# Kernel tuning notes

Measured on AMD Instinct MI355X. Metric: run time of the kernel, lower is better.

## Reference

```python
import jax, jax.numpy as jnp
import numpy as np

B, T, DIM = 32, 512, 512
Q, C, D = 8, 256, 256   # num_codebooks, nb_code, bottleneck_dim
HID = 1024
EPS = 1e-5


def _bn(h, gamma, beta):
    # BatchNorm1d (training mode): batch stats over all leading dims, biased var
    ax = tuple(range(h.ndim - 1))
    m = h.mean(axis=ax, keepdims=True)
    v = ((h - m) ** 2).mean(axis=ax, keepdims=True)
    return (h - m) / jnp.sqrt(v + EPS) * gamma + beta


def setup_inputs() -> dict:
    key = jax.random.key(0)
    ks = jax.random.split(key, 12)
    s = 0.02  # weight scale
    return {
        "x": jax.random.normal(ks[0], (B, DIM, T), jnp.float32),
        "u": jax.random.uniform(ks[1], (B, T, Q, C), jnp.float32),
        "codebook": jax.random.normal(ks[2], (Q, C, D), jnp.float32),
        "log_temps": jnp.zeros((Q,), jnp.float32),
        "enc_w0": jax.random.normal(ks[3], (HID, DIM), jnp.float32) * s,
        "enc_b0": jnp.zeros((HID,), jnp.float32),
        "enc_g0": jnp.ones((HID,), jnp.float32),
        "enc_be0": jnp.zeros((HID,), jnp.float32),
        "enc_w1": jax.random.normal(ks[4], (HID, HID), jnp.float32) * s,
        "enc_b1": jnp.zeros((HID,), jnp.float32),
        "enc_g1": jnp.ones((HID,), jnp.float32),
        "enc_be1": jnp.zeros((HID,), jnp.float32),
        "enc_wo": jax.random.normal(ks[5], (Q * D, HID), jnp.float32) * s,
        "enc_bo": jnp.zeros((Q * D,), jnp.float32),
        "dec_g": jnp.ones((D,), jnp.float32),
        "dec_be": jnp.zeros((D,), jnp.float32),
        "dec_w0": jax.random.normal(ks[6], (HID, D), jnp.float32) * s,
        "dec_b0": jnp.zeros((HID,), jnp.float32),
        "dec_g0": jnp.ones((HID,), jnp.float32),
        "dec_be0": jnp.zeros((HID,), jnp.float32),
        "dec_w1": jax.random.normal(ks[7], (HID, HID), jnp.float32) * s,
        "dec_b1": jnp.zeros((HID,), jnp.float32),
        "dec_g1": jnp.ones((HID,), jnp.float32),
        "dec_be1": jnp.zeros((HID,), jnp.float32),
        "fin_w": jax.random.normal(ks[8], (DIM, HID), jnp.float32) * s,
        "fin_b": jnp.zeros((DIM,), jnp.float32),
    }


def reference(x, u, codebook, log_temps,
              enc_w0, enc_b0, enc_g0, enc_be0,
              enc_w1, enc_b1, enc_g1, enc_be1,
              enc_wo, enc_bo,
              dec_g, dec_be,
              dec_w0, dec_b0, dec_g0, dec_be0,
              dec_w1, dec_b1, dec_g1, dec_be1,
              fin_w, fin_b):
    xt = jnp.swapaxes(x, 1, 2)  # b c t -> b t c

    # encoder: FFN(dim->hid->hid) + Linear(hid, Q*D)
    h = jax.nn.relu(_bn(xt @ enc_w0.T + enc_b0, enc_g0, enc_be0))
    h = jax.nn.relu(_bn(h @ enc_w1.T + enc_b1, enc_g1, enc_be1))
    z = (h @ enc_wo.T + enc_bo).reshape(B, T, Q, D)

    # multi-codebook logits
    logits_raw = jnp.einsum('btqd,qcd->btqc', z, codebook)  # [B,T,Q,C]
    indices = jnp.argmax(logits_raw, axis=-1)               # [B,T,Q]

    # per-codebook temperature scaling
    logits = logits_raw * jnp.exp(-log_temps)[:, None]

    # gumbel-softmax (tau=1, hard=True), gumbel noise from uniform u
    g = -jnp.log(-jnp.log(jnp.clip(u, 1e-9, 1.0)) + 1e-20)
    y_soft = jax.nn.softmax(logits + g, axis=-1)
    y_hard = jax.nn.one_hot(jnp.argmax(y_soft, axis=-1), C, dtype=y_soft.dtype)
    codes = y_hard - jax.lax.stop_gradient(y_soft) + y_soft  # straight-through

    # decoder: embed via codebook, batchnorm, FFN, final linear
    emb = codes.reshape(B, T, Q * C) @ codebook.reshape(Q * C, D)
    h = _bn(emb, dec_g, dec_be)
    h = jax.nn.relu(_bn(h @ dec_w0.T + dec_b0, dec_g0, dec_be0))
    h = jax.nn.relu(_bn(h @ dec_w1.T + dec_b1, dec_g1, dec_be1))
    x_reco = h @ fin_w.T + fin_b  # [B,T,DIM]

    commit_loss = jnp.mean((x_reco - xt) ** 2)
    return x_reco, indices, commit_loss
```

## Files before the change

kernel.cpp:

```cpp
#include <hip/hip_runtime.h>
#include <math.h>

#define BB   32
#define TT   512
#define DIM  512
#define HID  1024
#define QQ   8
#define CC   256
#define DD   256
#define BT   16384
#define EPSB 1e-5f

typedef _Float16 half4 __attribute__((ext_vector_type(4)));
typedef _Float16 half8 __attribute__((ext_vector_type(8)));
typedef float f32x4 __attribute__((ext_vector_type(4)));

#define GLOAD_LDS16(g, l)                                                      \
  __builtin_amdgcn_global_load_lds(                                            \
      (const __attribute__((address_space(1))) void*)(g),                      \
      (__attribute__((address_space(3))) void*)(l), 16, 0, 0)

#define S_BARRIER() asm volatile("s_barrier" ::: "memory")
#define S_VMCNT8()  asm volatile("s_waitcnt vmcnt(8)" ::: "memory")
#define S_VMCNT4()  asm volatile("s_waitcnt vmcnt(4)" ::: "memory")
#define S_VMCNT0()  asm volatile("s_waitcnt vmcnt(0)" ::: "memory")

__device__ inline void xcd_swizzle(int& bx, int& by) {
  int gx = gridDim.x, gy = gridDim.y;
  int h = blockIdx.x + gx * blockIdx.y;
  int c = h & 7, idx = h >> 3;
  bx = idx % gx;
  by = c * (gy >> 3) + idx / gx;
}

__global__ __launch_bounds__(256) void transpose_xt(const float* __restrict__ x,
                                                    float* __restrict__ xt,
                                                    _Float16* __restrict__ xhi,
                                                    _Float16* __restrict__ xlo) {
  __shared__ float tile[32][33];
  int tx = threadIdx.x, ty = threadIdx.y;
  int b = blockIdx.z;
  int t0 = blockIdx.x * 32, c0 = blockIdx.y * 32;
  const float* xb = x + (size_t)b * DIM * TT;
#pragma unroll
  for (int j = 0; j < 32; j += 8)
    tile[ty + j][tx] = xb[(size_t)(c0 + ty + j) * TT + (t0 + tx)];
  __syncthreads();
#pragma unroll
  for (int j = 0; j < 32; j += 8) {
    float v = tile[tx][ty + j];
    size_t gi = ((size_t)b * TT + t0 + ty + j) * DIM + (c0 + tx);
    xt[gi] = v;
    _Float16 h = (_Float16)v;
    xhi[gi] = h;
    xlo[gi] = (_Float16)(v - (float)h);
  }
}

__device__ inline void conv4(const float* __restrict__ in,
                             _Float16* __restrict__ o, int i) {
  float4 v = ((const float4*)in)[i];
  half4 hv;
  hv.x = (_Float16)v.x; hv.y = (_Float16)v.y;
  hv.z = (_Float16)v.z; hv.w = (_Float16)v.w;
  ((half4*)o)[i] = hv;
}

__device__ inline void split4(const float* __restrict__ in,
                              _Float16* __restrict__ hi,
                              _Float16* __restrict__ lo, int i, float scale) {
  float4 v = ((const float4*)in)[i];
  v.x *= scale; v.y *= scale; v.z *= scale; v.w *= scale;
  half4 hv, lv;
  hv.x = (_Float16)v.x; lv.x = (_Float16)(v.x - (float)hv.x);
  hv.y = (_Float16)v.y; lv.y = (_Float16)(v.y - (float)hv.y);
  hv.z = (_Float16)v.z; lv.z = (_Float16)(v.z - (float)hv.z);
  hv.w = (_Float16)v.w; lv.w = (_Float16)(v.w - (float)hv.w);
  ((half4*)hi)[i] = hv;
  ((half4*)lo)[i] = lv;
}

__global__ __launch_bounds__(256) void prep_weights(
    const float* __restrict__ dw0, const float* __restrict__ dw1,
    const float* __restrict__ fw, const float* __restrict__ ew0,
    const float* __restrict__ ew1, _Float16* __restrict__ w0h,
    _Float16* __restrict__ w1h, _Float16* __restrict__ wfh,
    _Float16* __restrict__ w0hi, _Float16* __restrict__ w0lo,
    _Float16* __restrict__ w1hi, _Float16* __restrict__ w1lo) {
  int b = blockIdx.x, t = threadIdx.x;
  if (b < 256) {
    conv4(dw0, w0h, b * 256 + t);
  } else if (b < 1280) {
    conv4(dw1, w1h, (b - 256) * 256 + t);
  } else if (b < 1792) {
    conv4(fw, wfh, (b - 1280) * 256 + t);
  } else if (b < 2304) {
    split4(ew0, w0hi, w0lo, (b - 1792) * 256 + t, 64.f);
  } else {
    split4(ew1, w1hi, w1lo, (b - 2304) * 256 + t, 64.f);
  }
}

__global__ __launch_bounds__(256) void fold_w(const float* __restrict__ cb,
                                              const float* __restrict__ wo,
                                              float* __restrict__ Wf) {
  __shared__ float As[8][128];
  __shared__ float Ws[8][128];
  const int tid = threadIdx.x;
  const int n0 = blockIdx.x * 128;
  const int m0 = blockIdx.y * 128;
  const int q = m0 >> 8;
  const int lr = tid >> 1, lk = (tid & 1) << 2;
  const float* Ap = cb + (size_t)q * CC * DD + (size_t)((m0 & 255) + lr) * DD + lk;
  const int br = tid >> 5, bc = (tid & 31) << 2;
  const float* Bp = wo + (size_t)(q * CC + br) * HID + n0 + bc;
  const int tm = (tid >> 4) << 3, tn = (tid & 15) << 3;

  float acc[8][8];
#pragma unroll
  for (int i = 0; i < 8; i++)
#pragma unroll
    for (int j = 0; j < 8; j++) acc[i][j] = 0.f;

  for (int kb = 0; kb < DD; kb += 8) {
    float4 av = *(const float4*)(Ap + kb);
    float4 bb = *(const float4*)(Bp + (size_t)kb * HID);
    __syncthreads();
    As[lk + 0][lr] = av.x; As[lk + 1][lr] = av.y;
    As[lk + 2][lr] = av.z; As[lk + 3][lr] = av.w;
    *(float4*)&Ws[br][bc] = bb;
    __syncthreads();
#pragma unroll
    for (int k = 0; k < 8; ++k) {
      float a[8], b[8];
      *(float4*)(a) = *(const float4*)(&As[k][tm]);
      *(float4*)(a + 4) = *(const float4*)(&As[k][tm + 4]);
      *(float4*)(b) = *(const float4*)(&Ws[k][tn]);
      *(float4*)(b + 4) = *(const float4*)(&Ws[k][tn + 4]);
#pragma unroll
      for (int i = 0; i < 8; i++)
#pragma unroll
        for (int j = 0; j < 8; j++) acc[i][j] = fmaf(a[i], b[j], acc[i][j]);
    }
  }
#pragma unroll
  for (int i = 0; i < 8; i++) {
    float* Cp = Wf + (size_t)(m0 + tm + i) * HID + (n0 + tn);
    float4 o;
    o.x = acc[i][0]; o.y = acc[i][1]; o.z = acc[i][2]; o.w = acc[i][3];
    *(float4*)Cp = o;
    o.x = acc[i][4]; o.y = acc[i][5]; o.z = acc[i][6]; o.w = acc[i][7];
    *(float4*)(Cp + 4) = o;
  }
}

__global__ __launch_bounds__(256) void fold_b(const float* __restrict__ cb,
                                              const float* __restrict__ bo,
                                              float* __restrict__ bf) {
  int q = blockIdx.x, c = threadIdx.x;
  const float* row = cb + ((size_t)q * CC + c) * DD;
  const float* b = bo + q * DD;
  float s = 0.f;
  for (int d = 0; d < DD; d++) s = fmaf(row[d], b[d], s);
  bf[q * CC + c] = s;
}

__global__ __launch_bounds__(256, 2) void hgemm3s_nt(
    const _Float16* __restrict__ Ahi, const _Float16* __restrict__ Alo,
    const _Float16* __restrict__ Whi, const _Float16* __restrict__ Wlo,
    const float* __restrict__ bias, float invsc, _Float16* __restrict__ Chi,
    _Float16* __restrict__ Clo, int ldc, int K, float* __restrict__ stats,
    int N) {
  __shared__ _Float16 Ah[2][4 * 128 * 8];
  __shared__ _Float16 Al[2][4 * 128 * 8];
  __shared__ _Float16 Bh[2][4 * 128 * 8];
  __shared__ _Float16 Bl[2][4 * 128 * 8];
  int BX, BY;
  xcd_swizzle(BX, BY);
  const int tid = threadIdx.x;
  const int l = tid & 63;
  const int w = tid >> 6;
  const int m0 = BY * 128, n0 = BX * 128;
  const int wrow = (w >> 1) * 64, wcol = (w & 1) * 64;

  const int s0 = tid, s1 = tid + 256;
  const int r0 = s0 & 127, kp0 = s0 >> 7;
  const int r1 = s1 & 127, kp1 = s1 >> 7;
  const size_t a0o = (size_t)(m0 + r0) * K + kp0 * 8;
  const size_t a1o = (size_t)(m0 + r1) * K + kp1 * 8;
  const size_t w0o = (size_t)(n0 + r0) * K + kp0 * 8;
  const size_t w1o = (size_t)(n0 + r1) * K + kp1 * 8;

  f32x4 acc[4][4] = {};

  auto stage = [&](int buf, int kb) {
    GLOAD_LDS16(Ahi + a0o + kb, &Ah[buf][s0 * 8]);
    GLOAD_LDS16(Ahi + a1o + kb, &Ah[buf][s1 * 8]);
    GLOAD_LDS16(Alo + a0o + kb, &Al[buf][s0 * 8]);
    GLOAD_LDS16(Alo + a1o + kb, &Al[buf][s1 * 8]);
    GLOAD_LDS16(Whi + w0o + kb, &Bh[buf][s0 * 8]);
    GLOAD_LDS16(Whi + w1o + kb, &Bh[buf][s1 * 8]);
    GLOAD_LDS16(Wlo + w0o + kb, &Bl[buf][s0 * 8]);
    GLOAD_LDS16(Wlo + w1o + kb, &Bl[buf][s1 * 8]);
  };
  auto compute = [&](int buf) {
    half8 ah[4], al[4], bh[4], bl[4];
#pragma unroll
    for (int i = 0; i < 4; i++) {
      const int idx = (((l >> 4) << 7) + wrow + i * 16 + (l & 15)) * 8;
      ah[i] = *(const half8*)&Ah[buf][idx];
      al[i] = *(const half8*)&Al[buf][idx];
    }
#pragma unroll
    for (int j = 0; j < 4; j++) {
      const int idx = (((l >> 4) << 7) + wcol + j * 16 + (l & 15)) * 8;
      bh[j] = *(const half8*)&Bh[buf][idx];
      bl[j] = *(const half8*)&Bl[buf][idx];
    }
#pragma unroll
    for (int i = 0; i < 4; i++)
#pragma unroll
      for (int j = 0; j < 4; j++) {
        acc[i][j] = __builtin_amdgcn_mfma_f32_16x16x32_f16(ah[i], bh[j],
                                                           acc[i][j], 0, 0, 0);
        acc[i][j] = __builtin_amdgcn_mfma_f32_16x16x32_f16(al[i], bh[j],
                                                           acc[i][j], 0, 0, 0);
        acc[i][j] = __builtin_amdgcn_mfma_f32_16x16x32_f16(ah[i], bl[j],
                                                           acc[i][j], 0, 0, 0);
      }
  };

  stage(0, 0);
  int cur = 0;
  for (int kb = 32; kb < K; kb += 32) {
    stage(cur ^ 1, kb);
    S_VMCNT8();
    S_BARRIER();
    compute(cur);
    S_BARRIER();
    cur ^= 1;
  }
  S_VMCNT0();
  S_BARRIER();
  compute(cur);

#pragma unroll
  for (int j = 0; j < 4; j++) {
    const int col = n0 + wcol + j * 16 + (l & 15);
    const float bb = bias[col];
    float s1v = 0.f, s2v = 0.f;
#pragma unroll
    for (int i = 0; i < 4; i++) {
#pragma unroll
      for (int r = 0; r < 4; r++) {
        float v = fmaf(acc[i][j][r], invsc, bb);
        const int row = m0 + wrow + i * 16 + ((l >> 4) << 2) + r;
        _Float16 hv = (_Float16)v;
        Chi[(size_t)row * ldc + col] = hv;
        Clo[(size_t)row * ldc + col] = (_Float16)(v - (float)hv);
        s1v += v;
        s2v = fmaf(v, v, s2v);
      }
    }
    s1v += __shfl_xor(s1v, 16); s1v += __shfl_xor(s1v, 32);
    s2v += __shfl_xor(s2v, 16); s2v += __shfl_xor(s2v, 32);
    if (l < 16) {
      atomicAdd(&stats[col], s1v);
      atomicAdd(&stats[N + col], s2v);
    }
  }
}

__global__ __launch_bounds__(512, 4) void hgemm3_wo_argmax(
    const _Float16* __restrict__ Ahi, const _Float16* __restrict__ Alo,
    const _Float16* __restrict__ Whi, const _Float16* __restrict__ Wlo,
    const float* __restrict__ bf, const float* __restrict__ u,
    const float* __restrict__ log_temps, float* __restrict__ out_idx,
    int* __restrict__ idx2) {
  __shared__ _Float16 Ahs[4 * 128 * 8];
  __shared__ _Float16 Als[4 * 128 * 8];
  __shared__ _Float16 Bhs[4 * 256 * 8];
  __shared__ _Float16 Bls[4 * 256 * 8];
  __shared__ float redv[2][128][4];
  __shared__ int   redi[2][128][4];
  int BX, BY;
  xcd_swizzle(BX, BY);
  const int tid = threadIdx.x;
  const int l = tid & 63;
  const int w = tid >> 6;
  const int q = BX;
  const int m0 = BY * 128;
  const int n0 = q * CC;
  const int wrow = (w >> 2) * 64, wcol = (w & 3) * 64;

  const int ar = tid & 127, akp = tid >> 7;
  const _Float16* Agh = Ahi + (size_t)(m0 + ar) * HID + akp * 8;
  const _Float16* Agl = Alo + (size_t)(m0 + ar) * HID + akp * 8;
  _Float16* Ahd = &Ahs[tid * 8];
  _Float16* Ald = &Als[tid * 8];
  const int s0 = tid, s1 = tid + 512;
  const int br0 = s0 & 255, bkp0 = s0 >> 8;
  const int br1 = s1 & 255, bkp1 = s1 >> 8;
  const _Float16* Bgh0 = Whi + (size_t)(n0 + br0) * HID + bkp0 * 8;
  const _Float16* Bgh1 = Whi + (size_t)(n0 + br1) * HID + bkp1 * 8;
  const _Float16* Bgl0 = Wlo + (size_t)(n0 + br0) * HID + bkp0 * 8;
  const _Float16* Bgl1 = Wlo + (size_t)(n0 + br1) * HID + bkp1 * 8;
  _Float16* Bhd0 = &Bhs[s0 * 8]; _Float16* Bhd1 = &Bhs[s1 * 8];
  _Float16* Bld0 = &Bls[s0 * 8]; _Float16* Bld1 = &Bls[s1 * 8];

  f32x4 acc[4][4] = {};

  for (int kb = 0; kb < HID; kb += 32) {
    __syncthreads();
    GLOAD_LDS16(Agh + kb, Ahd);
    GLOAD_LDS16(Agl + kb, Ald);
    GLOAD_LDS16(Bgh0 + kb, Bhd0);
    GLOAD_LDS16(Bgh1 + kb, Bhd1);
    GLOAD_LDS16(Bgl0 + kb, Bld0);
    GLOAD_LDS16(Bgl1 + kb, Bld1);
    __syncthreads();
    half8 ah[4], al[4], bh[4], bl[4];
#pragma unroll
    for (int i = 0; i < 4; i++) {
      const int idx = ((l >> 4) * 128 + wrow + i * 16 + (l & 15)) * 8;
      ah[i] = *(const half8*)&Ahs[idx];
      al[i] = *(const half8*)&Als[idx];
    }
#pragma unroll
    for (int j = 0; j < 4; j++) {
      const int idx = ((l >> 4) * 256 + wcol + j * 16 + (l & 15)) * 8;
      bh[j] = *(const half8*)&Bhs[idx];
      bl[j] = *(const half8*)&Bls[idx];
    }
#pragma unroll
    for (int i = 0; i < 4; i++)
#pragma unroll
      for (int j = 0; j < 4; j++) {
        acc[i][j] = __builtin_amdgcn_mfma_f32_16x16x32_f16(ah[i], bh[j],
                                                           acc[i][j], 0, 0, 0);
        acc[i][j] = __builtin_amdgcn_mfma_f32_16x16x32_f16(al[i], bh[j],
                                                           acc[i][j], 0, 0, 0);
        acc[i][j] = __builtin_amdgcn_mfma_f32_16x16x32_f16(ah[i], bl[j],
                                                           acc[i][j], 0, 0, 0);
      }
  }

  const float scale = expf(-log_temps[q]);
  float bcol[4];
#pragma unroll
  for (int j = 0; j < 4; j++) bcol[j] = bf[n0 + wcol + j * 16 + (l & 15)];

#pragma unroll
  for (int i = 0; i < 4; i++) {
#pragma unroll
    for (int r = 0; r < 4; r++) {
      const int rloc = wrow + i * 16 + ((l >> 4) << 2) + r;
      const int row = m0 + rloc;
      float bvv = -INFINITY; int bi = 0;
      float gv = -INFINITY; int gi = 0;
#pragma unroll
      for (int j = 0; j < 4; j++) {
        const int c = wcol + j * 16 + (l & 15);
        float v = acc[i][j][r] + bcol[j];
        if (v > bvv) { bvv = v; bi = c; }
        float uu = u[(size_t)row * (QQ * CC) + n0 + c];
        float uc = fminf(fmaxf(uu, 1e-9f), 1.0f);
        float g = -logf(-logf(uc) + 1e-20f);
        float y = fmaf(v, scale, g);
        if (y > gv) { gv = y; gi = c; }
      }
#pragma unroll
      for (int off = 1; off < 16; off <<= 1) {
        float b2 = __shfl_xor(bvv, off); int bi2 = __shfl_xor(bi, off);
        if (b2 > bvv || (b2 == bvv && bi2 < bi)) { bvv = b2; bi = bi2; }
        float g2 = __shfl_xor(gv, off); int gi2 = __shfl_xor(gi, off);
        if (g2 > gv || (g2 == gv && gi2 < gi)) { gv = g2; gi = gi2; }
      }
      if ((l & 15) == 0) {
        redv[0][rloc][w & 3] = bvv; redi[0][rloc][w & 3] = bi;
        redv[1][rloc][w & 3] = gv;  redi[1][rloc][w & 3] = gi;
      }
    }
  }
  __syncthreads();
  if (tid < 128) {
    float bv = redv[0][tid][0]; int bi = redi[0][tid][0];
    float gv = redv[1][tid][0]; int gi = redi[1][tid][0];
#pragma unroll
    for (int c = 1; c < 4; c++) {
      float v = redv[0][tid][c];
      if (v > bv) { bv = v; bi = redi[0][tid][c]; }
      float v2 = redv[1][tid][c];
      if (v2 > gv) { gv = v2; gi = redi[1][tid][c]; }
    }
    const int row = m0 + tid;
    out_idx[(size_t)row * QQ + q] = (float)bi;
    idx2[(size_t)row * QQ + q] = gi;
  }
}

__global__ __launch_bounds__(256, 2) void hgemm_ntf16(
    const _Float16* __restrict__ A, const _Float16* __restrict__ W,
    const float* __restrict__ bias, _Float16* __restrict__ C, int ldc, int K,
    float* __restrict__ stats, int N) {
  __shared__ _Float16 Al[2][4 * 128 * 8];
  __shared__ _Float16 Bl[2][4 * 128 * 8];
  int BX, BY;
  xcd_swizzle(BX, BY);
  const int tid = threadIdx.x;
  const int l = tid & 63;
  const int w = tid >> 6;
  const int m0 = BY * 128, n0 = BX * 128;
  const int wrow = (w >> 1) * 64, wcol = (w & 1) * 64;

  const int s0 = tid, s1 = tid + 256;
  const int r0 = s0 & 127, kp0 = s0 >> 7;
  const int r1 = s1 & 127, kp1 = s1 >> 7;
  const size_t a0o = (size_t)(m0 + r0) * K + kp0 * 8;
  const size_t a1o = (size_t)(m0 + r1) * K + kp1 * 8;
  const size_t w0o = (size_t)(n0 + r0) * K + kp0 * 8;
  const size_t w1o = (size_t)(n0 + r1) * K + kp1 * 8;

  f32x4 acc[4][4] = {};

  auto stage = [&](int buf, int kb) {
    GLOAD_LDS16(A + a0o + kb, &Al[buf][s0 * 8]);
    GLOAD_LDS16(A + a1o + kb, &Al[buf][s1 * 8]);
    GLOAD_LDS16(W + w0o + kb, &Bl[buf][s0 * 8]);
    GLOAD_LDS16(W + w1o + kb, &Bl[buf][s1 * 8]);
  };
  auto compute = [&](int buf) {
    half8 af[4], bfr[4];
#pragma unroll
    for (int i = 0; i < 4; i++)
      af[i] = *(const half8*)
          &Al[buf][(((l >> 4) << 7) + wrow + i * 16 + (l & 15)) * 8];
#pragma unroll
    for (int j = 0; j < 4; j++)
      bfr[j] = *(const half8*)
          &Bl[buf][(((l >> 4) << 7) + wcol + j * 16 + (l & 15)) * 8];
#pragma unroll
    for (int i = 0; i < 4; i++)
#pragma unroll
      for (int j = 0; j < 4; j++)
        acc[i][j] = __builtin_amdgcn_mfma_f32_16x16x32_f16(af[i], bfr[j],
                                                           acc[i][j], 0, 0, 0);
  };

  stage(0, 0);
  int cur = 0;
  for (int kb = 32; kb < K; kb += 32) {
    stage(cur ^ 1, kb);
    S_VMCNT4();
    S_BARRIER();
    compute(cur);
    S_BARRIER();
    cur ^= 1;
  }
  S_VMCNT0();
  S_BARRIER();
  compute(cur);

#pragma unroll
  for (int j = 0; j < 4; j++) {
    const int col = n0 + wcol + j * 16 + (l & 15);
    const float bb = bias[col];
    float s1v = 0.f, s2v = 0.f;
#pragma unroll
    for (int i = 0; i < 4; i++) {
#pragma unroll
      for (int r = 0; r < 4; r++) {
        float v = acc[i][j][r] + bb;
        const int row = m0 + wrow + i * 16 + ((l >> 4) << 2) + r;
        C[(size_t)row * ldc + col] = (_Float16)v;
        s1v += v;
        s2v = fmaf(v, v, s2v);
      }
    }
    s1v += __shfl_xor(s1v, 16); s1v += __shfl_xor(s1v, 32);
    s2v += __shfl_xor(s2v, 16); s2v += __shfl_xor(s2v, 32);
    if (l < 16) {
      atomicAdd(&stats[col], s1v);
      atomicAdd(&stats[N + col], s2v);
    }
  }
}

__global__ __launch_bounds__(256, 2) void hgemm_nt_loss(
    const _Float16* __restrict__ A, const _Float16* __restrict__ W,
    const float* __restrict__ bias, float* __restrict__ C, int ldc, int K,
    const float* __restrict__ xt, float* __restrict__ out_loss) {
  __shared__ _Float16 Al[2][4 * 128 * 8];
  __shared__ _Float16 Bl[2][4 * 128 * 8];
  int BX, BY;
  xcd_swizzle(BX, BY);
  const int tid = threadIdx.x;
  const int l = tid & 63;
  const int w = tid >> 6;
  const int m0 = BY * 128, n0 = BX * 128;
  const int wrow = (w >> 1) * 64, wcol = (w & 1) * 64;

  const int s0 = tid, s1 = tid + 256;
  const int r0 = s0 & 127, kp0 = s0 >> 7;
  const int r1 = s1 & 127, kp1 = s1 >> 7;
  const size_t a0o = (size_t)(m0 + r0) * K + kp0 * 8;
  const size_t a1o = (size_t)(m0 + r1) * K + kp1 * 8;
  const size_t w0o = (size_t)(n0 + r0) * K + kp0 * 8;
  const size_t w1o = (size_t)(n0 + r1) * K + kp1 * 8;

  f32x4 acc[4][4] = {};

  auto stage = [&](int buf, int kb) {
    GLOAD_LDS16(A + a0o + kb, &Al[buf][s0 * 8]);
    GLOAD_LDS16(A + a1o + kb, &Al[buf][s1 * 8]);
    GLOAD_LDS16(W + w0o + kb, &Bl[buf][s0 * 8]);
    GLOAD_LDS16(W + w1o + kb, &Bl[buf][s1 * 8]);
  };
  auto compute = [&](int buf) {
    half8 af[4], bfr[4];
#pragma unroll
    for (int i = 0; i < 4; i++)
      af[i] = *(const half8*)
          &Al[buf][(((l >> 4) << 7) + wrow + i * 16 + (l & 15)) * 8];
#pragma unroll
    for (int j = 0; j < 4; j++)
      bfr[j] = *(const half8*)
          &Bl[buf][(((l >> 4) << 7) + wcol + j * 16 + (l & 15)) * 8];
#pragma unroll
    for (int i = 0; i < 4; i++)
#pragma unroll
      for (int j = 0; j < 4; j++)
        acc[i][j] = __builtin_amdgcn_mfma_f32_16x16x32_f16(af[i], bfr[j],
                                                           acc[i][j], 0, 0, 0);
  };

  stage(0, 0);
  int cur = 0;
  for (int kb = 32; kb < K; kb += 32) {
    stage(cur ^ 1, kb);
    S_VMCNT4();
    S_BARRIER();
    compute(cur);
    S_BARRIER();
    cur ^= 1;
  }
  S_VMCNT0();
  S_BARRIER();
  compute(cur);

  float ls = 0.f;
#pragma unroll
  for (int j = 0; j < 4; j++) {
    const int col = n0 + wcol + j * 16 + (l & 15);
    const float bb = bias[col];
#pragma unroll
    for (int i = 0; i < 4; i++) {
#pragma unroll
      for (int r = 0; r < 4; r++) {
        float v = acc[i][j][r] + bb;
        const int row = m0 + wrow + i * 16 + ((l >> 4) << 2) + r;
        C[(size_t)row * ldc + col] = v;
        float d = v - xt[(size_t)row * ldc + col];
        ls = fmaf(d, d, ls);
      }
    }
  }
#pragma unroll
  for (int off = 32; off > 0; off >>= 1) ls += __shfl_xor(ls, off);
  if (l == 0)
    atomicAdd(out_loss, ls * (1.0f / ((float)BT * (float)DIM)));
}

__global__ __launch_bounds__(256) void bn_finalize(const float* __restrict__ sums,
                                                   const float* __restrict__ gamma,
                                                   const float* __restrict__ beta,
                                                   float* __restrict__ ss, int N) {
  int n = blockIdx.x * 256 + threadIdx.x;
  if (n >= N) return;
  const float invM = 1.0f / (float)BT;
  float mean = sums[n] * invM;
  float var = sums[N + n] * invM - mean * mean;
  float sc = gamma[n] / sqrtf(var + EPSB);
  ss[n] = sc;
  ss[N + n] = beta[n] - mean * sc;
}

__global__ __launch_bounds__(256) void bn_resplit(_Float16* __restrict__ hi,
                                                  _Float16* __restrict__ lo,
                                                  const float* __restrict__ ss,
                                                  int nmask, int N, long n4,
                                                  int relu) {
  long stride = (long)gridDim.x * 256;
  for (long i = (long)blockIdx.x * 256 + threadIdx.x; i < n4; i += stride) {
    int col = (int)((i << 2) & nmask);
    half4 h = ((half4*)hi)[i];
    half4 L = ((half4*)lo)[i];
    float4 sc = *(const float4*)(ss + col);
    float4 sh = *(const float4*)(ss + N + col);
    float vx = fmaf((float)h.x + (float)L.x, sc.x, sh.x);
    float vy = fmaf((float)h.y + (float)L.y, sc.y, sh.y);
    float vz = fmaf((float)h.z + (float)L.z, sc.z, sh.z);
    float vw = fmaf((float)h.w + (float)L.w, sc.w, sh.w);
    if (relu) {
      vx = fmaxf(vx, 0.f); vy = fmaxf(vy, 0.f);
      vz = fmaxf(vz, 0.f); vw = fmaxf(vw, 0.f);
    }
    half4 hv, lv;
    hv.x = (_Float16)vx; lv.x = (_Float16)(vx - (float)hv.x);
    hv.y = (_Float16)vy; lv.y = (_Float16)(vy - (float)hv.y);
    hv.z = (_Float16)vz; lv.z = (_Float16)(vz - (float)hv.z);
    hv.w = (_Float16)vw; lv.w = (_Float16)(vw - (float)hv.w);
    ((half4*)hi)[i] = hv;
    ((half4*)lo)[i] = lv;
  }
}

__global__ __launch_bounds__(256) void bnf16_inplace(_Float16* __restrict__ h,
                                                     const float* __restrict__ ss,
                                                     int nmask, int N, long n4,
                                                     int relu) {
  long stride = (long)gridDim.x * 256;
  for (long i = (long)blockIdx.x * 256 + threadIdx.x; i < n4; i += stride) {
    int col = (int)((i << 2) & nmask);
    half4 v = ((half4*)h)[i];
    float4 sc = *(const float4*)(ss + col);
    float4 sh = *(const float4*)(ss + N + col);
    float vx = fmaf((float)v.x, sc.x, sh.x);
    float vy = fmaf((float)v.y, sc.y, sh.y);
    float vz = fmaf((float)v.z, sc.z, sh.z);
    float vw = fmaf((float)v.w, sc.w, sh.w);
    if (relu) {
      vx = fmaxf(vx, 0.f); vy = fmaxf(vy, 0.f);
      vz = fmaxf(vz, 0.f); vw = fmaxf(vw, 0.f);
    }
    half4 o;
    o.x = (_Float16)vx; o.y = (_Float16)vy;
    o.z = (_Float16)vz; o.w = (_Float16)vw;
    ((half4*)h)[i] = o;
  }
}

__global__ __launch_bounds__(256) void bn_apply_f16(const float* __restrict__ h,
                                                    const float* __restrict__ ss,
                                                    int nmask, int N, long n4,
                                                    int relu,
                                                    _Float16* __restrict__ o) {
  long stride = (long)gridDim.x * 256;
  for (long i = (long)blockIdx.x * 256 + threadIdx.x; i < n4; i += stride) {
    int col = (int)((i << 2) & nmask);
    float4 v = ((const float4*)h)[i];
    float4 sc = *(const float4*)(ss + col);
    float4 sh = *(const float4*)(ss + N + col);
    v.x = fmaf(v.x, sc.x, sh.x); v.y = fmaf(v.y, sc.y, sh.y);
    v.z = fmaf(v.z, sc.z, sh.z); v.w = fmaf(v.w, sc.w, sh.w);
    if (relu) {
      v.x = fmaxf(v.x, 0.f); v.y = fmaxf(v.y, 0.f);
      v.z = fmaxf(v.z, 0.f); v.w = fmaxf(v.w, 0.f);
    }
    half4 hv;
    hv.x = (_Float16)v.x; hv.y = (_Float16)v.y;
    hv.z = (_Float16)v.z; hv.w = (_Float16)v.w;
    ((half4*)o)[i] = hv;
  }
}

__global__ __launch_bounds__(256) void conv_split_s(const float* __restrict__ in,
                                                    _Float16* __restrict__ hi,
                                                    _Float16* __restrict__ lo,
                                                    int n4, float scale) {
  int i = blockIdx.x * 256 + threadIdx.x;
  if (i >= n4) return;
  split4(in, hi, lo, i, scale);
}

__global__ __launch_bounds__(256) void emb_gather_stats(
    const float* __restrict__ cb, const int* __restrict__ idx2,
    float* __restrict__ emb, float* __restrict__ sums) {
  __shared__ int k[64][8];
  const int r0 = blockIdx.x * 64;
  const int tid = threadIdx.x;
  for (int t = tid; t < 64 * QQ; t += 256)
    k[t >> 3][t & 7] = idx2[(size_t)(r0 + (t >> 3)) * QQ + (t & 7)];
  __syncthreads();
  const int d = tid;
  float s1 = 0.f, s2 = 0.f;
  for (int rr = 0; rr < 64; rr++) {
    float s = 0.f;
#pragma unroll
    for (int q = 0; q < QQ; q++)
      s += cb[((size_t)(q * CC + k[rr][q])) * DD + d];
    emb[(size_t)(r0 + rr) * DD + d] = s;
    s1 += s;
    s2 = fmaf(s, s, s2);
  }
  atomicAdd(&sums[d], s1);
  atomicAdd(&sums[DD + d], s2);
}

static const size_t OF_XT = 0;
static const size_t OF_R1 = OF_XT + (size_t)BT * DIM;
static const size_t OF_R2 = OF_R1 + (size_t)BT * HID;
static const size_t OF_WF = OF_R2 + (size_t)BT * HID;
static const size_t OF_BF = OF_WF + (size_t)2048 * HID;
static const size_t OF_EMBH = OF_BF + 2048;
static const size_t OF_HB = OF_EMBH + (size_t)BT * DD / 2;
static const size_t OF_W0H = OF_HB + (size_t)BT * HID / 2;
static const size_t OF_W1H = OF_W0H + (size_t)HID * DD / 2;
static const size_t OF_WFH = OF_W1H + (size_t)HID * HID / 2;
static const size_t OF_I2 = OF_WFH + (size_t)DIM * HID / 2;
static const size_t OF_ST = OF_I2 + (size_t)BT * QQ;
static const size_t OF_SS0 = OF_ST + 4096;
static const size_t OF_SS1 = OF_SS0 + 2048;
static const size_t OF_SSD = OF_SS1 + 2048;
static const size_t OF_SD0 = OF_SSD + 1024;
static const size_t OF_SD1 = OF_SD0 + 2048;

extern "C" void kernel_launch(void* const* d_in, const int* in_sizes, int n_in,
                              void* d_out, int out_size, void* d_ws, size_t ws_size,
                              hipStream_t stream) {
  const float* x        = (const float*)d_in[0];
  const float* u        = (const float*)d_in[1];
  const float* codebook = (const float*)d_in[2];
  const float* log_temps= (const float*)d_in[3];
  const float* enc_w0   = (const float*)d_in[4];
  const float* enc_b0   = (const float*)d_in[5];
  const float* enc_g0   = (const float*)d_in[6];
  const float* enc_be0  = (const float*)d_in[7];
  const float* enc_w1   = (const float*)d_in[8];
  const float* enc_b1   = (const float*)d_in[9];
  const float* enc_g1   = (const float*)d_in[10];
  const float* enc_be1  = (const float*)d_in[11];
  const float* enc_wo   = (const float*)d_in[12];
  const float* enc_bo   = (const float*)d_in[13];
  const float* dec_g    = (const float*)d_in[14];
  const float* dec_be   = (const float*)d_in[15];
  const float* dec_w0   = (const float*)d_in[16];
  const float* dec_b0   = (const float*)d_in[17];
  const float* dec_g0   = (const float*)d_in[18];
  const float* dec_be0  = (const float*)d_in[19];
  const float* dec_w1   = (const float*)d_in[20];
  const float* dec_b1   = (const float*)d_in[21];
  const float* dec_g1   = (const float*)d_in[22];
  const float* dec_be1  = (const float*)d_in[23];
  const float* fin_w    = (const float*)d_in[24];
  const float* fin_b    = (const float*)d_in[25];

  float* ws = (float*)d_ws;
  float* xt = ws + OF_XT;
  float* R1 = ws + OF_R1;
  float* Wf = ws + OF_WF;
  float* bfold = ws + OF_BF;
  _Float16* embh = (_Float16*)(ws + OF_EMBH);
  _Float16* w0h = (_Float16*)(ws + OF_W0H);
  _Float16* w1h = (_Float16*)(ws + OF_W1H);
  _Float16* wfh = (_Float16*)(ws + OF_WFH);
  int* idx2 = (int*)(ws + OF_I2);
  float* st = ws + OF_ST;
  float* ss0 = ws + OF_SS0;
  float* ss1 = ws + OF_SS1;
  float* ssd = ws + OF_SSD;
  float* sd0 = ws + OF_SD0;
  float* sd1 = ws + OF_SD1;

  _Float16* xthi = (_Float16*)(ws + OF_R2);
  _Float16* xtlo = (_Float16*)(ws + OF_R2 + (size_t)BT * DIM / 2);
  _Float16* w0hi = (_Float16*)(ws + OF_R2 + (size_t)BT * DIM);
  _Float16* w0lo = (_Float16*)(ws + OF_R2 + (size_t)BT * DIM + (size_t)HID * DIM / 2);
  _Float16* w1hi = (_Float16*)(ws + OF_R2 + (size_t)BT * DIM + (size_t)HID * DIM);
  _Float16* w1lo = (_Float16*)(ws + OF_R2 + (size_t)BT * DIM + (size_t)HID * DIM +
                               (size_t)HID * HID / 2);
  _Float16* r1hi = (_Float16*)(ws + OF_R1);
  _Float16* r1lo = (_Float16*)(ws + OF_R1 + (size_t)BT * HID / 2);
  _Float16* r2hi = (_Float16*)(ws + OF_HB);
  _Float16* r2lo = (_Float16*)(ws + OF_R2);
  _Float16* wfhi = (_Float16*)(ws + OF_R1);
  _Float16* wflo = (_Float16*)(ws + OF_R1 + (size_t)2048 * HID / 2);
  _Float16* h16a = (_Float16*)(ws + OF_R2);
  _Float16* h16b = (_Float16*)(ws + OF_R2 + (size_t)BT * HID / 2);

  float* out = (float*)d_out;
  float* out_idx = out + (size_t)BT * DIM;
  float* out_loss = out + (size_t)BT * DIM + (size_t)BT * QQ;

  hipMemsetAsync(out_loss, 0, sizeof(float), stream);

  prep_weights<<<dim3(3328), 256, 0, stream>>>(
      dec_w0, dec_w1, fin_w, enc_w0, enc_w1, w0h, w1h, wfh, w0hi, w0lo, w1hi,
      w1lo);
  fold_w<<<dim3(HID / 128, 2048 / 128), 256, 0, stream>>>(codebook, enc_wo, Wf);
  fold_b<<<dim3(QQ), 256, 0, stream>>>(codebook, enc_bo, bfold);

  transpose_xt<<<dim3(TT / 32, DIM / 32, BB), dim3(32, 8), 0, stream>>>(
      x, xt, xthi, xtlo);

  hipMemsetAsync(st, 0, 2 * HID * sizeof(float), stream);
  hgemm3s_nt<<<dim3(HID / 128, BT / 128), 256, 0, stream>>>(
      xthi, xtlo, w0hi, w0lo, enc_b0, 1.f / 64.f, r1hi, r1lo, HID, DIM, st, HID);
  bn_finalize<<<dim3(4), 256, 0, stream>>>(st, enc_g0, enc_be0, ss0, HID);
  bn_resplit<<<dim3(2048), 256, 0, stream>>>(r1hi, r1lo, ss0, HID - 1, HID,
                                             (long)BT * HID / 4, 1);

  hipMemsetAsync(st, 0, 2 * HID * sizeof(float), stream);
  hgemm3s_nt<<<dim3(HID / 128, BT / 128), 256, 0, stream>>>(
      r1hi, r1lo, w1hi, w1lo, enc_b1, 1.f / 64.f, r2hi, r2lo, HID, HID, st, HID);
  conv_split_s<<<dim3(2048 * HID / 4 / 256), 256, 0, stream>>>(
      Wf, wfhi, wflo, 2048 * HID / 4, 1.f);
  bn_finalize<<<dim3(4), 256, 0, stream>>>(st, enc_g1, enc_be1, ss1, HID);
  bn_resplit<<<dim3(2048), 256, 0, stream>>>(r2hi, r2lo, ss1, HID - 1, HID,
                                             (long)BT * HID / 4, 1);

  hgemm3_wo_argmax<<<dim3(QQ, BT / 128), 512, 0, stream>>>(
      r2hi, r2lo, wfhi, wflo, bfold, u, log_temps, out_idx, idx2);

  hipMemsetAsync(st, 0, 2 * DD * sizeof(float), stream);
  emb_gather_stats<<<dim3(BT / 64), 256, 0, stream>>>(codebook, idx2, R1, st);
  bn_finalize<<<dim3(1), 256, 0, stream>>>(st, dec_g, dec_be, ssd, DD);
  bn_apply_f16<<<dim3(2048), 256, 0, stream>>>(R1, ssd, DD - 1, DD,
                                               (long)BT * DD / 4, 0, embh);

  hipMemsetAsync(st, 0, 2 * HID * sizeof(float), stream);
  hgemm_ntf16<<<dim3(HID / 128, BT / 128), 256, 0, stream>>>(
      embh, w0h, dec_b0, h16a, HID, DD, st, HID);
  bn_finalize<<<dim3(4), 256, 0, stream>>>(st, dec_g0, dec_be0, sd0, HID);
  bnf16_inplace<<<dim3(2048), 256, 0, stream>>>(h16a, sd0, HID - 1, HID,
                                                (long)BT * HID / 4, 1);

  hipMemsetAsync(st, 0, 2 * HID * sizeof(float), stream);
  hgemm_ntf16<<<dim3(HID / 128, BT / 128), 256, 0, stream>>>(
      h16a, w1h, dec_b1, h16b, HID, HID, st, HID);
  bn_finalize<<<dim3(4), 256, 0, stream>>>(st, dec_g1, dec_be1, sd1, HID);
  bnf16_inplace<<<dim3(2048), 256, 0, stream>>>(h16b, sd1, HID - 1, HID,
                                                (long)BT * HID / 4, 1);

  hgemm_nt_loss<<<dim3(DIM / 128, BT / 128), 256, 0, stream>>>(
      h16b, wfh, fin_b, out, DIM, HID, xt, out_loss);
}
```

Measured before the change: 1.163 ms.

## Double-buffer codebook-logit GEMM with 128x128 tiles and split argmax reduction

Replaces the single-buffered 128x256-tile fused GEMM+argmax kernel with a 128x128-tile, 256-thread kernel. It double-buffers LDS loads via global_load_lds and waits with vmcnt, so loads overlap the MFMA work. Each codebook's 256 columns are now split across two blocks, each writing a partial argmax value and index, and a small second kernel merges the two halves. This trades an extra launch and the partial-result traffic for load/compute overlap and more blocks. The merge breaks ties toward the first half, which keeps the lowest-index tie rule.

```diff
diff --git a/kernel.cpp b/kernel.cpp
--- a/kernel.cpp
+++ b/kernel.cpp
@@ -271,66 +271,62 @@
   }
 }
 
-__global__ __launch_bounds__(512, 4) void hgemm3_wo_argmax(
+__global__ __launch_bounds__(256, 2) void hgemm3s_wo_part(
     const _Float16* __restrict__ Ahi, const _Float16* __restrict__ Alo,
     const _Float16* __restrict__ Whi, const _Float16* __restrict__ Wlo,
     const float* __restrict__ bf, const float* __restrict__ u,
-    const float* __restrict__ log_temps, float* __restrict__ out_idx,
-    int* __restrict__ idx2) {
-  __shared__ _Float16 Ahs[4 * 128 * 8];
-  __shared__ _Float16 Als[4 * 128 * 8];
-  __shared__ _Float16 Bhs[4 * 256 * 8];
-  __shared__ _Float16 Bls[4 * 256 * 8];
-  __shared__ float redv[2][128][4];
-  __shared__ int   redi[2][128][4];
+    const float* __restrict__ log_temps, float* __restrict__ pval,
+    int* __restrict__ pidx) {
+  __shared__ _Float16 Ah[2][4 * 128 * 8];
+  __shared__ _Float16 Al[2][4 * 128 * 8];
+  __shared__ _Float16 Bh[2][4 * 128 * 8];
+  __shared__ _Float16 Bl[2][4 * 128 * 8];
+  __shared__ float redv[2][128][2];
+  __shared__ int   redi[2][128][2];
   int BX, BY;
   xcd_swizzle(BX, BY);
   const int tid = threadIdx.x;
   const int l = tid & 63;
   const int w = tid >> 6;
-  const int q = BX;
-  const int m0 = BY * 128;
-  const int n0 = q * CC;
-  const int wrow = (w >> 2) * 64, wcol = (w & 3) * 64;
-
-  const int ar = tid & 127, akp = tid >> 7;
-  const _Float16* Agh = Ahi + (size_t)(m0 + ar) * HID + akp * 8;
-  const _Float16* Agl = Alo + (size_t)(m0 + ar) * HID + akp * 8;
-  _Float16* Ahd = &Ahs[tid * 8];
-  _Float16* Ald = &Als[tid * 8];
-  const int s0 = tid, s1 = tid + 512;
-  const int br0 = s0 & 255, bkp0 = s0 >> 8;
-  const int br1 = s1 & 255, bkp1 = s1 >> 8;
-  const _Float16* Bgh0 = Whi + (size_t)(n0 + br0) * HID + bkp0 * 8;
-  const _Float16* Bgh1 = Whi + (size_t)(n0 + br1) * HID + bkp1 * 8;
-  const _Float16* Bgl0 = Wlo + (size_t)(n0 + br0) * HID + bkp0 * 8;
-  const _Float16* Bgl1 = Wlo + (size_t)(n0 + br1) * HID + bkp1 * 8;
-  _Float16* Bhd0 = &Bhs[s0 * 8]; _Float16* Bhd1 = &Bhs[s1 * 8];
-  _Float16* Bld0 = &Bls[s0 * 8]; _Float16* Bld1 = &Bls[s1 * 8];
+  const int m0 = BY * 128, n0 = BX * 128;
+  const int q = n0 >> 8;
+  const int half = (n0 >> 7) & 1;
+  const int wrow = (w >> 1) * 64, wcol = (w & 1) * 64;
+  const int K = HID;
+
+  const int s0 = tid, s1 = tid + 256;
+  const int r0 = s0 & 127, kp0 = s0 >> 7;
+  const int r1 = s1 & 127, kp1 = s1 >> 7;
+  const size_t a0o = (size_t)(m0 + r0) * K + kp0 * 8;
+  const size_t a1o = (size_t)(m0 + r1) * K + kp1 * 8;
+  const size_t w0o = (size_t)(n0 + r0) * K + kp0 * 8;
+  const size_t w1o = (size_t)(n0 + r1) * K + kp1 * 8;
 
   f32x4 acc[4][4] = {};
 
-  for (int kb = 0; kb < HID; kb += 32) {
-    __syncthreads();
-    GLOAD_LDS16(Agh + kb, Ahd);
-    GLOAD_LDS16(Agl + kb, Ald);
-    GLOAD_LDS16(Bgh0 + kb, Bhd0);
-    GLOAD_LDS16(Bgh1 + kb, Bhd1);
-    GLOAD_LDS16(Bgl0 + kb, Bld0);
-    GLOAD_LDS16(Bgl1 + kb, Bld1);
-    __syncthreads();
+  auto stage = [&](int buf, int kb) {
+    GLOAD_LDS16(Ahi + a0o + kb, &Ah[buf][s0 * 8]);
+    GLOAD_LDS16(Ahi + a1o + kb, &Ah[buf][s1 * 8]);
+    GLOAD_LDS16(Alo + a0o + kb, &Al[buf][s0 * 8]);
+    GLOAD_LDS16(Alo + a1o + kb, &Al[buf][s1 * 8]);
+    GLOAD_LDS16(Whi + w0o + kb, &Bh[buf][s0 * 8]);
+    GLOAD_LDS16(Whi + w1o + kb, &Bh[buf][s1 * 8]);
+    GLOAD_LDS16(Wlo + w0o + kb, &Bl[buf][s0 * 8]);
+    GLOAD_LDS16(Wlo + w1o + kb, &Bl[buf][s1 * 8]);
+  };
+  auto compute = [&](int buf) {
     half8 ah[4], al[4], bh[4], bl[4];
 #pragma unroll
     for (int i = 0; i < 4; i++) {
-      const int idx = ((l >> 4) * 128 + wrow + i * 16 + (l & 15)) * 8;
-      ah[i] = *(const half8*)&Ahs[idx];
-      al[i] = *(const half8*)&Als[idx];
+      const int idx = (((l >> 4) << 7) + wrow + i * 16 + (l & 15)) * 8;
+      ah[i] = *(const half8*)&Ah[buf][idx];
+      al[i] = *(const half8*)&Al[buf][idx];
     }
 #pragma unroll
     for (int j = 0; j < 4; j++) {
-      const int idx = ((l >> 4) * 256 + wcol + j * 16 + (l & 15)) * 8;
-      bh[j] = *(const half8*)&Bhs[idx];
-      bl[j] = *(const half8*)&Bls[idx];
+      const int idx = (((l >> 4) << 7) + wcol + j * 16 + (l & 15)) * 8;
+      bh[j] = *(const half8*)&Bh[buf][idx];
+      bl[j] = *(const half8*)&Bl[buf][idx];
     }
 #pragma unroll
     for (int i = 0; i < 4; i++)
@@ -343,7 +339,21 @@
         acc[i][j] = __builtin_amdgcn_mfma_f32_16x16x32_f16(ah[i], bl[j],
                                                            acc[i][j], 0, 0, 0);
       }
-  }
+  };
+
+  stage(0, 0);
+  int cur = 0;
+  for (int kb = 32; kb < K; kb += 32) {
+    stage(cur ^ 1, kb);
+    S_VMCNT8();
+    S_BARRIER();
+    compute(cur);
+    S_BARRIER();
+    cur ^= 1;
+  }
+  S_VMCNT0();
+  S_BARRIER();
+  compute(cur);
 
   const float scale = expf(-log_temps[q]);
   float bcol[4];
@@ -360,10 +370,10 @@
       float gv = -INFINITY; int gi = 0;
 #pragma unroll
       for (int j = 0; j < 4; j++) {
-        const int c = wcol + j * 16 + (l & 15);
+        const int c = (n0 & 255) + wcol + j * 16 + (l & 15);
         float v = acc[i][j][r] + bcol[j];
         if (v > bvv) { bvv = v; bi = c; }
-        float uu = u[(size_t)row * (QQ * CC) + n0 + c];
+        float uu = u[(size_t)row * (QQ * CC) + n0 + wcol + j * 16 + (l & 15)];
         float uc = fminf(fmaxf(uu, 1e-9f), 1.0f);
         float g = -logf(-logf(uc) + 1e-20f);
         float y = fmaf(v, scale, g);
@@ -377,25 +387,43 @@
         if (g2 > gv || (g2 == gv && gi2 < gi)) { gv = g2; gi = gi2; }
       }
       if ((l & 15) == 0) {
-        redv[0][rloc][w & 3] = bvv; redi[0][rloc][w & 3] = bi;
-        redv[1][rloc][w & 3] = gv;  redi[1][rloc][w & 3] = gi;
+        redv[0][rloc][w & 1] = bvv; redi[0][rloc][w & 1] = bi;
+        redv[1][rloc][w & 1] = gv;  redi[1][rloc][w & 1] = gi;
       }
     }
   }
   __syncthreads();
   if (tid < 128) {
     float bv = redv[0][tid][0]; int bi = redi[0][tid][0];
+    {
+      float v = redv[0][tid][1]; int ii = redi[0][tid][1];
+      if (v > bv || (v == bv && ii < bi)) { bv = v; bi = ii; }
+    }
     float gv = redv[1][tid][0]; int gi = redi[1][tid][0];
-#pragma unroll
-    for (int c = 1; c < 4; c++) {
-      float v = redv[0][tid][c];
-      if (v > bv) { bv = v; bi = redi[0][tid][c]; }
-      float v2 = redv[1][tid][c];
-      if (v2 > gv) { gv = v2; gi = redi[1][tid][c]; }
-    }
-    const int row = m0 + tid;
-    out_idx[(size_t)row * QQ + q] = (float)bi;
-    idx2[(size_t)row * QQ + q] = gi;
+    {
+      float v = redv[1][tid][1]; int ii = redi[1][tid][1];
+      if (v > gv || (v == gv && ii < gi)) { gv = v; gi = ii; }
+    }
+    const size_t base = (((size_t)(m0 + tid) * QQ + q) << 1) + half;
+    const size_t toff = (size_t)BT * QQ * 2;
+    pval[base] = bv;        pidx[base] = bi;
+    pval[toff + base] = gv; pidx[toff + base] = gi;
+  }
+}
+
+__global__ __launch_bounds__(256) void argmax_reduce(
+    const float* __restrict__ pval, const int* __restrict__ pidx,
+    float* __restrict__ out_idx, int* __restrict__ idx2) {
+  int i = blockIdx.x * 256 + threadIdx.x;
+  if (i >= BT * QQ) return;
+  {
+    float v0 = pval[2 * i], v1 = pval[2 * i + 1];
+    out_idx[i] = (float)((v1 > v0) ? pidx[2 * i + 1] : pidx[2 * i]);
+  }
+  {
+    const size_t off = (size_t)BT * QQ * 2;
+    float v0 = pval[off + 2 * i], v1 = pval[off + 2 * i + 1];
+    idx2[i] = (v1 > v0) ? pidx[off + 2 * i + 1] : pidx[off + 2 * i];
   }
 }
 
@@ -777,6 +805,8 @@
   _Float16* wflo = (_Float16*)(ws + OF_R1 + (size_t)2048 * HID / 2);
   _Float16* h16a = (_Float16*)(ws + OF_R2);
   _Float16* h16b = (_Float16*)(ws + OF_R2 + (size_t)BT * HID / 2);
+  float* pval = ws + OF_WF;
+  int* pidx = (int*)(ws + OF_WF + (size_t)2 * BT * QQ * 2);
 
   float* out = (float*)d_out;
   float* out_idx = out + (size_t)BT * DIM;
@@ -809,8 +839,10 @@
   bn_resplit<<<dim3(2048), 256, 0, stream>>>(r2hi, r2lo, ss1, HID - 1, HID,
                                              (long)BT * HID / 4, 1);
 
-  hgemm3_wo_argmax<<<dim3(QQ, BT / 128), 512, 0, stream>>>(
-      r2hi, r2lo, wfhi, wflo, bfold, u, log_temps, out_idx, idx2);
+  hgemm3s_wo_part<<<dim3(2048 / 128, BT / 128), 256, 0, stream>>>(
+      r2hi, r2lo, wfhi, wflo, bfold, u, log_temps, pval, pidx);
+  argmax_reduce<<<dim3(BT * QQ / 256), 256, 0, stream>>>(pval, pidx, out_idx,
+                                                         idx2);
 
   hipMemsetAsync(st, 0, 2 * DD * sizeof(float), stream);
   emb_gather_stats<<<dim3(BT / 64), 256, 0, stream>>>(codebook, idx2, R1, st);
```

New measurement: 1.187 ms. Within noise of the previous version (+2.0%).
